# Kernel tuning notes

Hardware: AMD Instinct MI355X
Metric: run time of the kernel (lower is better)

The kernel has to match this reference:

```python
import jax, jax.numpy as jnp
import numpy as np

TOKENS, D_IN, D_OUT, N_FACTORS, RANK = 8192, 4096, 4096, 2, 64


def setup_inputs() -> dict:
    key = jax.random.key(0)
    ks = jax.random.split(key, 6)
    # kaiming_uniform-ish scales (exact init distribution is irrelevant for correctness)
    w_bound = 1.0 / np.sqrt(D_IN)
    x = jax.random.normal(ks[0], (TOKENS, D_IN), dtype=jnp.float32)
    W = jax.random.uniform(ks[1], (D_OUT, D_IN), jnp.float32, -w_bound, w_bound)
    bias = jax.random.uniform(ks[2], (D_OUT,), jnp.float32, -w_bound, w_bound)
    a_bound = 1.0 / np.sqrt(RANK)
    As = jax.random.uniform(ks[3], (N_FACTORS, D_OUT, RANK), jnp.float32, -a_bound, a_bound)
    Bs = jax.random.normal(ks[4], (N_FACTORS, RANK, RANK), dtype=jnp.float32) * 0.1
    # Cs initialized nonzero here so the low-rank path actually contributes
    Cs = jax.random.normal(ks[5], (N_FACTORS, RANK, D_IN), dtype=jnp.float32) * 0.02
    return {"x": x, "W": W, "bias": bias, "As": As, "Bs": Bs, "Cs": Cs}


def reference(x, W, bias, As, Bs, Cs):
    # W_eff = W + sum_f tanh(A_f) @ B_f @ C_f   (phi_A = tanh, B already transformed)
    # [f,o,r] x [f,r,k] -> [f,o,k]; then x [f,k,i] -> [o,i] summed over f
    AB = jnp.einsum('for,frk->fok', jnp.tanh(As), Bs)
    W_eff = W + jnp.einsum('fok,fki->oi', AB, Cs)
    # F.linear: x @ W_eff^T + bias
    return jnp.einsum('ti,oi->to', x, W_eff) + bias
```

## Files before the change

kernel.cpp:

```cpp
#include <hip/hip_runtime.h>
#include <hip/hip_bf16.h>

typedef __bf16 bf16x8 __attribute__((ext_vector_type(8)));
typedef float f32x4 __attribute__((ext_vector_type(4)));

#define TOKENS 8192
#define D_IN   4096
#define D_OUT  4096

static __device__ __forceinline__ unsigned short f2bf(float f) {
  union { float f; unsigned int u; } v; v.f = f;
  unsigned int r = v.u + 0x7FFFu + ((v.u >> 16) & 1u);
  return (unsigned short)(r >> 16);
}

__global__ void ab_kernel(const float* __restrict__ As,
                          const float* __restrict__ Bs,
                          float* __restrict__ ABt) {
  __shared__ float tA[4][64];
  __shared__ float sB[64][64];
  const int t = threadIdx.x;
  const int f = blockIdx.x >> 10;
  const int o0 = (blockIdx.x & 1023) * 4;
  const int ol = t >> 6;
  const int k  = t & 63;
  tA[ol][k] = tanhf(As[((size_t)f * 4096 + o0 + ol) * 64 + k]);
#pragma unroll
  for (int j = 0; j < 16; ++j) {
    int e = t + 256 * j;
    sB[e >> 6][e & 63] = Bs[f * 4096 + e];
  }
  __syncthreads();
  float acc = 0.f;
#pragma unroll
  for (int r = 0; r < 64; ++r) acc += tA[ol][r] * sB[r][k];
  ABt[(size_t)(o0 + ol) * 128 + f * 64 + k] = acc;
}

__global__ void weff_kernel(const float* __restrict__ W,
                            const float* __restrict__ ABt,
                            const float* __restrict__ Cs,
                            unsigned short* __restrict__ Weff) {
  __shared__ float sA[64][129];
  __shared__ float sB[32][64];
  const int t = threadIdx.x;
  const int i0 = blockIdx.x * 64;
  const int o0 = blockIdx.y * 64;
#pragma unroll
  for (int j = 0; j < 32; ++j) {
    int e = t + 256 * j;
    sA[e >> 7][e & 127] = ABt[(size_t)(o0 + (e >> 7)) * 128 + (e & 127)];
  }
  const int tx = t & 15, ty = t >> 4;
  float acc[4][4] = {};
  for (int kc = 0; kc < 128; kc += 32) {
    __syncthreads();
#pragma unroll
    for (int j = 0; j < 8; ++j) {
      int e = t + 256 * j;
      sB[e >> 6][e & 63] = Cs[(size_t)(kc + (e >> 6)) * D_IN + i0 + (e & 63)];
    }
    __syncthreads();
#pragma unroll
    for (int k = 0; k < 32; ++k) {
      float4 b = *(const float4*)&sB[k][tx * 4];
#pragma unroll
      for (int r = 0; r < 4; ++r) {
        float a = sA[ty * 4 + r][kc + k];
        acc[r][0] += a * b.x;
        acc[r][1] += a * b.y;
        acc[r][2] += a * b.z;
        acc[r][3] += a * b.w;
      }
    }
  }
#pragma unroll
  for (int r = 0; r < 4; ++r) {
    const int o = o0 + ty * 4 + r;
    const float4 w = *(const float4*)&W[(size_t)o * D_IN + i0 + tx * 4];
    union { unsigned short h[4]; uint2 u; } p;
    p.h[0] = f2bf(w.x + acc[r][0]);
    p.h[1] = f2bf(w.y + acc[r][1]);
    p.h[2] = f2bf(w.z + acc[r][2]);
    p.h[3] = f2bf(w.w + acc[r][3]);
    *(uint2*)(Weff + (size_t)o * D_IN + i0 + tx * 4) = p.u;
  }
}

__global__ void cast_kernel(const float* __restrict__ x,
                            unsigned short* __restrict__ xb) {
  size_t i = ((size_t)blockIdx.x * 256 + threadIdx.x) * 8;
  float4 a = *(const float4*)(x + i);
  float4 b = *(const float4*)(x + i + 4);
  union { unsigned short h[8]; uint4 u; } p;
  p.h[0] = f2bf(a.x); p.h[1] = f2bf(a.y);
  p.h[2] = f2bf(a.z); p.h[3] = f2bf(a.w);
  p.h[4] = f2bf(b.x); p.h[5] = f2bf(b.y);
  p.h[6] = f2bf(b.z); p.h[7] = f2bf(b.w);
  *(uint4*)(xb + i) = p.u;
}

__global__ __launch_bounds__(256) void gemm_kernel(
    const unsigned short* __restrict__ Abf,
    const unsigned short* __restrict__ Bbf,
    const float* __restrict__ bias,
    float* __restrict__ C) {
  const int K = D_IN, N = D_OUT;
  __shared__ __align__(16) unsigned short sA[128 * 64];
  __shared__ __align__(16) unsigned short sB[128 * 64];
  const int t = threadIdx.x;
  const int lane = t & 63;
  const int wave = t >> 6;
  const int bn = blockIdx.x, bm = blockIdx.y;
  const int wm = (wave & 1) * 64, wn = (wave >> 1) * 64;

  const int r8 = (t >> 3) & 7;
  const int cg = (t & 7) ^ r8;
  const unsigned short* ag = Abf + (size_t)(bm * 128 + (t >> 3)) * K + cg * 8;
  const unsigned short* bg = Bbf + (size_t)(bn * 128 + (t >> 3)) * K + cg * 8;
  unsigned short* la = sA + t * 8;
  unsigned short* lb = sB + t * 8;

  f32x4 acc[4][4] = {};
  const int lm = lane & 15;
  const int cb = lane >> 4;
  const int sw = lm & 7;

  for (int kt = 0; kt < K; kt += 64) {
    __syncthreads();
#pragma unroll
    for (int j = 0; j < 4; ++j) {
      __builtin_amdgcn_global_load_lds(
          (const __attribute__((address_space(1))) void*)(ag + (size_t)j * 32 * K + kt),
          (__attribute__((address_space(3))) void*)(la + j * 2048), 16, 0, 0);
      __builtin_amdgcn_global_load_lds(
          (const __attribute__((address_space(1))) void*)(bg + (size_t)j * 32 * K + kt),
          (__attribute__((address_space(3))) void*)(lb + j * 2048), 16, 0, 0);
    }
    __syncthreads();
#pragma unroll
    for (int ks = 0; ks < 2; ++ks) {
      const int ch = ((ks * 4 + cb) ^ sw) * 8;
      bf16x8 af[4], bfr[4];
#pragma unroll
      for (int mi = 0; mi < 4; ++mi)
        af[mi] = *(const bf16x8*)(sA + (wm + mi * 16 + lm) * 64 + ch);
#pragma unroll
      for (int ni = 0; ni < 4; ++ni)
        bfr[ni] = *(const bf16x8*)(sB + (wn + ni * 16 + lm) * 64 + ch);
#pragma unroll
      for (int mi = 0; mi < 4; ++mi)
#pragma unroll
        for (int ni = 0; ni < 4; ++ni)
          acc[mi][ni] = __builtin_amdgcn_mfma_f32_16x16x32_bf16(
              af[mi], bfr[ni], acc[mi][ni], 0, 0, 0);
    }
  }

  const int cn = lane & 15;
  const int rm = (lane >> 4) * 4;
#pragma unroll
  for (int ni = 0; ni < 4; ++ni) {
    const int col = bn * 128 + wn + ni * 16 + cn;
    const float bv = bias[col];
#pragma unroll
    for (int mi = 0; mi < 4; ++mi) {
      const int row0 = bm * 128 + wm + mi * 16 + rm;
#pragma unroll
      for (int r = 0; r < 4; ++r)
        C[(size_t)(row0 + r) * N + col] = acc[mi][ni][r] + bv;
    }
  }
}

extern "C" void kernel_launch(void* const* d_in, const int* in_sizes, int n_in,
                              void* d_out, int out_size, void* d_ws, size_t ws_size,
                              hipStream_t stream) {
  const float* x    = (const float*)d_in[0];
  const float* W    = (const float*)d_in[1];
  const float* bias = (const float*)d_in[2];
  const float* As   = (const float*)d_in[3];
  const float* Bs   = (const float*)d_in[4];
  const float* Cs   = (const float*)d_in[5];
  float* out = (float*)d_out;

  char* ws = (char*)d_ws;
  float* ABt           = (float*)ws;
  unsigned short* Weff = (unsigned short*)(ws + (2u << 20));
  unsigned short* xb   = (unsigned short*)(ws + (2u << 20) + (32u << 20));

  ab_kernel<<<2048, 256, 0, stream>>>(As, Bs, ABt);
  weff_kernel<<<dim3(64, 64), 256, 0, stream>>>(W, ABt, Cs, Weff);
  cast_kernel<<<16384, 256, 0, stream>>>(x, xb);
  gemm_kernel<<<dim3(32, 64), 256, 0, stream>>>(xb, Weff, bias, out);
}
```

Baseline: 600.2 us.

## Rewrite bf16 GEMM as 256x256 tile, 8-wave, double-buffered pipelined kernel

Replaces the 128x128 single-buffered GEMM with a 256x256 tile computed by 8 waves, double-buffered LDS, and interleaved global-to-LDS prefetches issued between MFMA quadrants with explicit waitcnt, barriers and setprio. It also adds workgroup-index swizzling for L2 locality. The goal is to hide global load latency behind MFMA work and raise arithmetic intensity per tile. In exchange it uses more LDS (128KB) and registers and depends on hand-tuned wait counts for correctness.

New measurement: 570.0 us. 5.0% less time.

```diff
diff --git a/kernel.cpp b/kernel.cpp
--- a/kernel.cpp
+++ b/kernel.cpp
@@ -100,72 +100,210 @@
   *(uint4*)(xb + i) = p.u;
 }
 
-__global__ __launch_bounds__(256) void gemm_kernel(
+
+#define FENCE()   asm volatile("" ::: "memory")
+#define BARRIER() do { FENCE(); __builtin_amdgcn_s_barrier(); FENCE(); } while (0)
+#define WAITLGKM() asm volatile("s_waitcnt lgkmcnt(0)" ::: "memory")
+#define WAITVM(n)  asm volatile("s_waitcnt vmcnt(" #n ")" ::: "memory")
+#define SCHEDB()   __builtin_amdgcn_sched_barrier(0)
+
+#define GLOAD(gptr, lptr)                                                     \
+  __builtin_amdgcn_global_load_lds(                                           \
+      (const __attribute__((address_space(1))) void*)(gptr),                  \
+      (__attribute__((address_space(3))) void*)(lptr), 16, 0, 0)
+
+#define STAGE_A(buf, h, kt) do {                                              \
+    GLOAD(ag + (size_t)((h) * 128) * K + (kt),                                \
+          lA + (buf) * 16384 + (h) * 8192);                                   \
+    GLOAD(ag + (size_t)((h) * 128 + 64) * K + (kt),                           \
+          lA + (buf) * 16384 + (h) * 8192 + 4096);                            \
+  } while (0)
+#define STAGE_B(buf, h, kt) do {                                              \
+    GLOAD(bg + (size_t)((h) * 128) * K + (kt),                                \
+          lB + (buf) * 16384 + (h) * 8192);                                   \
+    GLOAD(bg + (size_t)((h) * 128 + 64) * K + (kt),                           \
+          lB + (buf) * 16384 + (h) * 8192 + 4096);                            \
+  } while (0)
+
+#define LDA(buf, mi, ks) \
+  (*(const bf16x8*)(rA + (buf) * 16384 + (mi) * 1024 + ((ks) ? ch1 : ch0)))
+#define LDB(buf, ni, ks) \
+  (*(const bf16x8*)(rB + (buf) * 16384 + (ni) * 1024 + ((ks) ? ch1 : ch0)))
+
+#define MFMA1(d, a, b) \
+  (d) = __builtin_amdgcn_mfma_f32_16x16x32_bf16((a), (b), (d), 0, 0, 0)
+
+#define QUADRANT(q, A00, A01, A10, A11)                                       \
+    MFMA1(acc[2*(q)  ][0], A00, b00);                                         \
+    MFMA1(acc[2*(q)+1][0], A10, b00);                                         \
+    MFMA1(acc[2*(q)  ][1], A00, b10);                                         \
+    MFMA1(acc[2*(q)+1][1], A10, b10);                                         \
+    MFMA1(acc[2*(q)  ][2], A00, b20);                                         \
+    MFMA1(acc[2*(q)+1][2], A10, b20);                                         \
+    MFMA1(acc[2*(q)  ][3], A00, b30);                                         \
+    MFMA1(acc[2*(q)+1][3], A10, b30);                                         \
+    MFMA1(acc[2*(q)  ][0], A01, b01);                                         \
+    MFMA1(acc[2*(q)+1][0], A11, b01);                                         \
+    MFMA1(acc[2*(q)  ][1], A01, b11);                                         \
+    MFMA1(acc[2*(q)+1][1], A11, b11);                                         \
+    MFMA1(acc[2*(q)  ][2], A01, b21);                                         \
+    MFMA1(acc[2*(q)+1][2], A11, b21);                                         \
+    MFMA1(acc[2*(q)  ][3], A01, b31);                                         \
+    MFMA1(acc[2*(q)+1][3], A11, b31);
+
+#define GEMM_BODY(S2, S3, kt)                                                 \
+  {                                                                           \
+    bf16x8 b00, b01, b10, b11, b20, b21, b30, b31;                            \
+                        \
+    {                                                                 \
+      bf16x8 a00 = LDA(0, 0, 0), a01 = LDA(0, 0, 1);                          \
+      bf16x8 a10 = LDA(0, 1, 0), a11 = LDA(0, 1, 1);                          \
+      b00 = LDB(0, 0, 0); b01 = LDB(0, 0, 1);                                 \
+      b10 = LDB(0, 1, 0); b11 = LDB(0, 1, 1);                                 \
+      b20 = LDB(0, 2, 0); b21 = LDB(0, 2, 1);                                 \
+      b30 = LDB(0, 3, 0); b31 = LDB(0, 3, 1);                                 \
+      STAGE_A(1, 0, (kt) + 64);                                               \
+      BARRIER(); WAITLGKM(); SCHEDB();                                        \
+      __builtin_amdgcn_s_setprio(1);                                          \
+      QUADRANT(0, a00, a01, a10, a11);                                        \
+      __builtin_amdgcn_s_setprio(0);                                          \
+      BARRIER();                                                              \
+    }                                                                         \
+    {                                                                 \
+      bf16x8 a00 = LDA(0, 2, 0), a01 = LDA(0, 2, 1);                          \
+      bf16x8 a10 = LDA(0, 3, 0), a11 = LDA(0, 3, 1);                          \
+      STAGE_A(1, 1, (kt) + 64);                                               \
+      if (S2) STAGE_B(0, 0, (kt) + 128);                                      \
+      BARRIER(); WAITLGKM(); SCHEDB();                                        \
+      __builtin_amdgcn_s_setprio(1);                                          \
+      QUADRANT(1, a00, a01, a10, a11);                                        \
+      __builtin_amdgcn_s_setprio(0);                                          \
+      BARRIER();                                                              \
+    }                                                                         \
+    {                                                                 \
+      bf16x8 a00 = LDA(0, 4, 0), a01 = LDA(0, 4, 1);                          \
+      bf16x8 a10 = LDA(0, 5, 0), a11 = LDA(0, 5, 1);                          \
+      if (S2) STAGE_B(0, 1, (kt) + 128);                                      \
+      BARRIER(); WAITLGKM(); SCHEDB();                                        \
+      __builtin_amdgcn_s_setprio(1);                                          \
+      QUADRANT(2, a00, a01, a10, a11);                                        \
+      __builtin_amdgcn_s_setprio(0);                                          \
+      BARRIER();                                                              \
+    }                                                                         \
+    {                                                                 \
+      bf16x8 a00 = LDA(0, 6, 0), a01 = LDA(0, 6, 1);                          \
+      bf16x8 a10 = LDA(0, 7, 0), a11 = LDA(0, 7, 1);                          \
+      BARRIER(); WAITLGKM(); SCHEDB();                                        \
+      __builtin_amdgcn_s_setprio(1);                                          \
+      QUADRANT(3, a00, a01, a10, a11);                                        \
+      __builtin_amdgcn_s_setprio(0);                                          \
+      if (S2) { WAITVM(4); } else { WAITVM(0); }                              \
+      BARRIER();                                                              \
+    }                                                                         \
+                      \
+    {                                                                 \
+      bf16x8 a00 = LDA(1, 0, 0), a01 = LDA(1, 0, 1);                          \
+      bf16x8 a10 = LDA(1, 1, 0), a11 = LDA(1, 1, 1);                          \
+      b00 = LDB(1, 0, 0); b01 = LDB(1, 0, 1);                                 \
+      b10 = LDB(1, 1, 0); b11 = LDB(1, 1, 1);                                 \
+      b20 = LDB(1, 2, 0); b21 = LDB(1, 2, 1);                                 \
+      b30 = LDB(1, 3, 0); b31 = LDB(1, 3, 1);                                 \
+      if (S2) STAGE_A(0, 0, (kt) + 128);                                      \
+      BARRIER(); WAITLGKM(); SCHEDB();                                        \
+      __builtin_amdgcn_s_setprio(1);                                          \
+      QUADRANT(0, a00, a01, a10, a11);                                        \
+      __builtin_amdgcn_s_setprio(0);                                          \
+      BARRIER();                                                              \
+    }                                                                         \
+    {                                                                 \
+      bf16x8 a00 = LDA(1, 2, 0), a01 = LDA(1, 2, 1);                          \
+      bf16x8 a10 = LDA(1, 3, 0), a11 = LDA(1, 3, 1);                          \
+      if (S2) STAGE_A(0, 1, (kt) + 128);                                      \
+      if (S3) STAGE_B(1, 0, (kt) + 192);                                      \
+      BARRIER(); WAITLGKM(); SCHEDB();                                        \
+      __builtin_amdgcn_s_setprio(1);                                          \
+      QUADRANT(1, a00, a01, a10, a11);                                        \
+      __builtin_amdgcn_s_setprio(0);                                          \
+      BARRIER();                                                              \
+    }                                                                         \
+    {                                                                 \
+      bf16x8 a00 = LDA(1, 4, 0), a01 = LDA(1, 4, 1);                          \
+      bf16x8 a10 = LDA(1, 5, 0), a11 = LDA(1, 5, 1);                          \
+      if (S3) STAGE_B(1, 1, (kt) + 192);                                      \
+      BARRIER(); WAITLGKM(); SCHEDB();                                        \
+      __builtin_amdgcn_s_setprio(1);                                          \
+      QUADRANT(2, a00, a01, a10, a11);                                        \
+      __builtin_amdgcn_s_setprio(0);                                          \
+      BARRIER();                                                              \
+    }                                                                         \
+    {                                                                 \
+      bf16x8 a00 = LDA(1, 6, 0), a01 = LDA(1, 6, 1);                          \
+      bf16x8 a10 = LDA(1, 7, 0), a11 = LDA(1, 7, 1);                          \
+      BARRIER(); WAITLGKM(); SCHEDB();                                        \
+      __builtin_amdgcn_s_setprio(1);                                          \
+      QUADRANT(3, a00, a01, a10, a11);                                        \
+      __builtin_amdgcn_s_setprio(0);                                          \
+      if (S3) { WAITVM(4); } else { WAITVM(0); }                              \
+      BARRIER();                                                              \
+    }                                                                         \
+  }
+
+__global__ __launch_bounds__(512, 2) void gemm_kernel(
     const unsigned short* __restrict__ Abf,
     const unsigned short* __restrict__ Bbf,
     const float* __restrict__ bias,
     float* __restrict__ C) {
   const int K = D_IN, N = D_OUT;
-  __shared__ __align__(16) unsigned short sA[128 * 64];
-  __shared__ __align__(16) unsigned short sB[128 * 64];
+  __shared__ __align__(16) unsigned short sA[2 * 256 * 64];
+  __shared__ __align__(16) unsigned short sB[2 * 256 * 64];
   const int t = threadIdx.x;
   const int lane = t & 63;
   const int wave = t >> 6;
-  const int bn = blockIdx.x, bm = blockIdx.y;
-  const int wm = (wave & 1) * 64, wn = (wave >> 1) * 64;
-
-  const int r8 = (t >> 3) & 7;
-  const int cg = (t & 7) ^ r8;
-  const unsigned short* ag = Abf + (size_t)(bm * 128 + (t >> 3)) * K + cg * 8;
-  const unsigned short* bg = Bbf + (size_t)(bn * 128 + (t >> 3)) * K + cg * 8;
-  unsigned short* la = sA + t * 8;
-  unsigned short* lb = sB + t * 8;
-
-  f32x4 acc[4][4] = {};
+
+  const int wgid = blockIdx.y * gridDim.x + blockIdx.x;
+  const int swz = (wgid & 7) * 64 + (wgid >> 3);
+  const int bn = swz & 15;
+  const int bm = swz >> 4;
+
+  const int wm = (wave >> 2) * 128;
+  const int wn = (wave & 3) * 64;
+
+  const int tr = t >> 3;
+  const int cg = (t & 7) ^ (tr & 7);
+  const unsigned short* ag = Abf + (size_t)(bm * 256 + tr) * K + cg * 8;
+  const unsigned short* bg = Bbf + (size_t)(bn * 256 + tr) * K + cg * 8;
+  unsigned short* const lA = sA + t * 8;
+  unsigned short* const lB = sB + t * 8;
+
   const int lm = lane & 15;
   const int cb = lane >> 4;
   const int sw = lm & 7;
-
-  for (int kt = 0; kt < K; kt += 64) {
-    __syncthreads();
-#pragma unroll
-    for (int j = 0; j < 4; ++j) {
-      __builtin_amdgcn_global_load_lds(
-          (const __attribute__((address_space(1))) void*)(ag + (size_t)j * 32 * K + kt),
-          (__attribute__((address_space(3))) void*)(la + j * 2048), 16, 0, 0);
-      __builtin_amdgcn_global_load_lds(
-          (const __attribute__((address_space(1))) void*)(bg + (size_t)j * 32 * K + kt),
-          (__attribute__((address_space(3))) void*)(lb + j * 2048), 16, 0, 0);
-    }
-    __syncthreads();
-#pragma unroll
-    for (int ks = 0; ks < 2; ++ks) {
-      const int ch = ((ks * 4 + cb) ^ sw) * 8;
-      bf16x8 af[4], bfr[4];
-#pragma unroll
-      for (int mi = 0; mi < 4; ++mi)
-        af[mi] = *(const bf16x8*)(sA + (wm + mi * 16 + lm) * 64 + ch);
-#pragma unroll
-      for (int ni = 0; ni < 4; ++ni)
-        bfr[ni] = *(const bf16x8*)(sB + (wn + ni * 16 + lm) * 64 + ch);
-#pragma unroll
-      for (int mi = 0; mi < 4; ++mi)
-#pragma unroll
-        for (int ni = 0; ni < 4; ++ni)
-          acc[mi][ni] = __builtin_amdgcn_mfma_f32_16x16x32_bf16(
-              af[mi], bfr[ni], acc[mi][ni], 0, 0, 0);
-    }
-  }
+  const int ch0 = ((cb) ^ sw) * 8;
+  const int ch1 = ((4 + cb) ^ sw) * 8;
+  const unsigned short* rA = sA + (wm + lm) * 64;
+  const unsigned short* rB = sB + (wn + lm) * 64;
+
+  f32x4 acc[8][4] = {};
+
+  STAGE_B(0, 0, 0); STAGE_B(0, 1, 0);
+  STAGE_A(0, 0, 0); STAGE_A(0, 1, 0);
+  STAGE_B(1, 0, 64); STAGE_B(1, 1, 64);
+  WAITVM(4);
+  BARRIER();
+
+#pragma unroll 1
+  for (int kt = 0; kt < K - 128; kt += 128) GEMM_BODY(1, 1, kt)
+  GEMM_BODY(0, 0, K - 128)
 
   const int cn = lane & 15;
   const int rm = (lane >> 4) * 4;
 #pragma unroll
   for (int ni = 0; ni < 4; ++ni) {
-    const int col = bn * 128 + wn + ni * 16 + cn;
+    const int col = bn * 256 + wn + ni * 16 + cn;
     const float bv = bias[col];
 #pragma unroll
-    for (int mi = 0; mi < 4; ++mi) {
-      const int row0 = bm * 128 + wm + mi * 16 + rm;
+    for (int mi = 0; mi < 8; ++mi) {
+      const int row0 = bm * 256 + wm + mi * 16 + rm;
 #pragma unroll
       for (int r = 0; r < 4; ++r)
         C[(size_t)(row0 + r) * N + col] = acc[mi][ni][r] + bv;
@@ -192,5 +330,5 @@
   ab_kernel<<<2048, 256, 0, stream>>>(As, Bs, ABt);
   weff_kernel<<<dim3(64, 64), 256, 0, stream>>>(W, ABt, Cs, Weff);
   cast_kernel<<<16384, 256, 0, stream>>>(x, xb);
-  gemm_kernel<<<dim3(32, 64), 256, 0, stream>>>(xb, Weff, bias, out);
-}
+  gemm_kernel<<<dim3(16, 32), 512, 0, stream>>>(xb, Weff, bias, out);
+}
```

## Rewrite GEMM as 256x256 tile, 8-wave, double-buffered pipelined MFMA kernel

Applied to the files above, without the earlier changes.

Replaces the 128x128 single-buffered bf16 GEMM with a 256x256 tile processed by 512 threads. The LDS buffers are double-buffered and global-to-LDS loads are interleaved with MFMA quads through explicit barriers, vmcnt waits, sched barriers and setprio. Workgroup IDs are remapped for L2 locality. The aim is to hide global load latency and raise MFMA utilization. In exchange it uses 128KB of LDS and many registers, and the hand-scheduled waits and barriers are fragile.

Result: faster. 565.5 us (-5.8%).

```diff
diff --git a/kernel.cpp b/kernel.cpp
--- a/kernel.cpp
+++ b/kernel.cpp
@@ -100,72 +100,183 @@
   *(uint4*)(xb + i) = p.u;
 }
 
-__global__ __launch_bounds__(256) void gemm_kernel(
+
+#define FENCE()   asm volatile("" ::: "memory")
+#define BARRIER() do { FENCE(); __builtin_amdgcn_s_barrier(); FENCE(); } while (0)
+#define WAITVM(n)  asm volatile("s_waitcnt vmcnt(" #n ")" ::: "memory")
+#define SCHEDB()   __builtin_amdgcn_sched_barrier(0)
+#define PRIO1      __builtin_amdgcn_s_setprio(1)
+#define PRIO0      __builtin_amdgcn_s_setprio(0)
+
+#define GLOAD(gptr, lptr)                                                     \
+  __builtin_amdgcn_global_load_lds(                                           \
+      (const __attribute__((address_space(1))) void*)(gptr),                  \
+      (__attribute__((address_space(3))) void*)(lptr), 16, 0, 0)
+
+#define STAGE_A(buf, h, kt) do {                                              \
+    GLOAD(ag + (size_t)((h) * 128) * K + (kt),                                \
+          lA + (buf) * 16384 + (h) * 8192);                                   \
+    GLOAD(ag + (size_t)((h) * 128 + 64) * K + (kt),                           \
+          lA + (buf) * 16384 + (h) * 8192 + 4096);                            \
+  } while (0)
+#define STAGE_B(buf, h, kt) do {                                              \
+    GLOAD(bg + (size_t)((h) * 128) * K + (kt),                                \
+          lB + (buf) * 16384 + (h) * 8192);                                   \
+    GLOAD(bg + (size_t)((h) * 128 + 64) * K + (kt),                           \
+          lB + (buf) * 16384 + (h) * 8192 + 4096);                            \
+  } while (0)
+
+#define LDA(buf, mi, ks) \
+  (*(const bf16x8*)(rA + (buf) * 16384 + (mi) * 1024 + ((ks) ? ch1 : ch0)))
+#define LDB(buf, ni, ks) \
+  (*(const bf16x8*)(rB + (buf) * 16384 + (ni) * 1024 + ((ks) ? ch1 : ch0)))
+
+#define READ_A(R0, R1, R2, R3, buf, mi0) do {                                 \
+    R0 = LDA(buf, (mi0), 0);                                                  \
+    R2 = LDA(buf, (mi0) + 1, 0);                                              \
+    R1 = LDA(buf, (mi0), 1);                                                  \
+    R3 = LDA(buf, (mi0) + 1, 1);                                              \
+  } while (0)
+#define READ_B(buf) do {                                                      \
+    b00 = LDB(buf, 0, 0); b10 = LDB(buf, 1, 0);                               \
+    b20 = LDB(buf, 2, 0); b30 = LDB(buf, 3, 0);                               \
+    b01 = LDB(buf, 0, 1); b11 = LDB(buf, 1, 1);                               \
+    b21 = LDB(buf, 2, 1); b31 = LDB(buf, 3, 1);                               \
+  } while (0)
+
+#define MFMA1(d, a, b) \
+  (d) = __builtin_amdgcn_mfma_f32_16x16x32_bf16((a), (b), (d), 0, 0, 0)
+
+#define QUAD(q, A0, A1, A2, A3)                                               \
+    MFMA1(acc[2*(q)  ][0], A0, b00);                                          \
+    MFMA1(acc[2*(q)+1][0], A2, b00);                                          \
+    MFMA1(acc[2*(q)  ][1], A0, b10);                                          \
+    MFMA1(acc[2*(q)+1][1], A2, b10);                                          \
+    MFMA1(acc[2*(q)  ][2], A0, b20);                                          \
+    MFMA1(acc[2*(q)+1][2], A2, b20);                                          \
+    MFMA1(acc[2*(q)  ][3], A0, b30);                                          \
+    MFMA1(acc[2*(q)+1][3], A2, b30);                                          \
+    MFMA1(acc[2*(q)  ][0], A1, b01);                                          \
+    MFMA1(acc[2*(q)+1][0], A3, b01);                                          \
+    MFMA1(acc[2*(q)  ][1], A1, b11);                                          \
+    MFMA1(acc[2*(q)+1][1], A3, b11);                                          \
+    MFMA1(acc[2*(q)  ][2], A1, b21);                                          \
+    MFMA1(acc[2*(q)+1][2], A3, b21);                                          \
+    MFMA1(acc[2*(q)  ][3], A1, b31);                                          \
+    MFMA1(acc[2*(q)+1][3], A3, b31);
+
+#define GEMM_BODY(S2, S3, kt)                                                 \
+  {                                                                           \
+                             \
+    READ_B(0);                                                                \
+    READ_A(qa0, qa1, qa2, qa3, 0, 2);                                         \
+    STAGE_A(1, 0, (kt) + 64); STAGE_A(1, 1, (kt) + 64);                       \
+    BARRIER(); SCHEDB();                                                      \
+    PRIO1; QUAD(0, pa0, pa1, pa2, pa3); PRIO0; SCHEDB();                      \
+    BARRIER();                                                                \
+                                          \
+    READ_A(pa0, pa1, pa2, pa3, 0, 4);                                         \
+    if (S2) { STAGE_B(0, 0, (kt) + 128); STAGE_B(0, 1, (kt) + 128); }         \
+    BARRIER(); SCHEDB();                                                      \
+    PRIO1; QUAD(1, qa0, qa1, qa2, qa3); PRIO0; SCHEDB();                      \
+    BARRIER();                                                                \
+                         \
+    READ_A(qa0, qa1, qa2, qa3, 0, 6);                                         \
+    BARRIER(); SCHEDB();                                                      \
+    PRIO1; QUAD(2, pa0, pa1, pa2, pa3); PRIO0; SCHEDB();                      \
+    if (S2) { WAITVM(4); } else { WAITVM(0); }                                \
+    BARRIER();                                                                \
+                                  \
+    READ_A(pa0, pa1, pa2, pa3, 1, 0);                                         \
+    BARRIER(); SCHEDB();                                                      \
+    PRIO1; QUAD(3, qa0, qa1, qa2, qa3); PRIO0; SCHEDB();                      \
+    BARRIER();                                                                \
+                               \
+    READ_B(1);                                                                \
+    READ_A(qa0, qa1, qa2, qa3, 1, 2);                                         \
+    if (S2) { STAGE_A(0, 0, (kt) + 128); STAGE_A(0, 1, (kt) + 128); }         \
+    BARRIER(); SCHEDB();                                                      \
+    PRIO1; QUAD(0, pa0, pa1, pa2, pa3); PRIO0; SCHEDB();                      \
+    BARRIER();                                                                \
+                                        \
+    READ_A(pa0, pa1, pa2, pa3, 1, 4);                                         \
+    if (S3) { STAGE_B(1, 0, (kt) + 192); STAGE_B(1, 1, (kt) + 192); }         \
+    BARRIER(); SCHEDB();                                                      \
+    PRIO1; QUAD(1, qa0, qa1, qa2, qa3); PRIO0; SCHEDB();                      \
+    BARRIER();                                                                \
+                       \
+    READ_A(qa0, qa1, qa2, qa3, 1, 6);                                         \
+    BARRIER(); SCHEDB();                                                      \
+    PRIO1; QUAD(2, pa0, pa1, pa2, pa3); PRIO0; SCHEDB();                      \
+    if (S3) { WAITVM(4); } else { WAITVM(0); }                                \
+    BARRIER();                                                                \
+                                  \
+    if (S2) { READ_A(pa0, pa1, pa2, pa3, 0, 0); }                             \
+    BARRIER(); SCHEDB();                                                      \
+    PRIO1; QUAD(3, qa0, qa1, qa2, qa3); PRIO0; SCHEDB();                      \
+    BARRIER();                                                                \
+  }
+
+__global__ __launch_bounds__(512, 2) void gemm_kernel(
     const unsigned short* __restrict__ Abf,
     const unsigned short* __restrict__ Bbf,
     const float* __restrict__ bias,
     float* __restrict__ C) {
   const int K = D_IN, N = D_OUT;
-  __shared__ __align__(16) unsigned short sA[128 * 64];
-  __shared__ __align__(16) unsigned short sB[128 * 64];
+  __shared__ __align__(16) unsigned short sA[2 * 256 * 64];
+  __shared__ __align__(16) unsigned short sB[2 * 256 * 64];
   const int t = threadIdx.x;
   const int lane = t & 63;
   const int wave = t >> 6;
-  const int bn = blockIdx.x, bm = blockIdx.y;
-  const int wm = (wave & 1) * 64, wn = (wave >> 1) * 64;
-
-  const int r8 = (t >> 3) & 7;
-  const int cg = (t & 7) ^ r8;
-  const unsigned short* ag = Abf + (size_t)(bm * 128 + (t >> 3)) * K + cg * 8;
-  const unsigned short* bg = Bbf + (size_t)(bn * 128 + (t >> 3)) * K + cg * 8;
-  unsigned short* la = sA + t * 8;
-  unsigned short* lb = sB + t * 8;
-
-  f32x4 acc[4][4] = {};
+
+  const int wgid = blockIdx.y * gridDim.x + blockIdx.x;
+  const int swz = (wgid & 7) * 64 + (wgid >> 3);
+  const int bn = swz & 15;
+  const int bm = swz >> 4;
+
+  const int wm = (wave >> 2) * 128;
+  const int wn = (wave & 3) * 64;
+
+  const int tr = t >> 3;
+  const int cg = (t & 7) ^ (tr & 7);
+  const unsigned short* ag = Abf + (size_t)(bm * 256 + tr) * K + cg * 8;
+  const unsigned short* bg = Bbf + (size_t)(bn * 256 + tr) * K + cg * 8;
+  unsigned short* const lA = sA + t * 8;
+  unsigned short* const lB = sB + t * 8;
+
   const int lm = lane & 15;
   const int cb = lane >> 4;
   const int sw = lm & 7;
-
-  for (int kt = 0; kt < K; kt += 64) {
-    __syncthreads();
-#pragma unroll
-    for (int j = 0; j < 4; ++j) {
-      __builtin_amdgcn_global_load_lds(
-          (const __attribute__((address_space(1))) void*)(ag + (size_t)j * 32 * K + kt),
-          (__attribute__((address_space(3))) void*)(la + j * 2048), 16, 0, 0);
-      __builtin_amdgcn_global_load_lds(
-          (const __attribute__((address_space(1))) void*)(bg + (size_t)j * 32 * K + kt),
-          (__attribute__((address_space(3))) void*)(lb + j * 2048), 16, 0, 0);
-    }
-    __syncthreads();
-#pragma unroll
-    for (int ks = 0; ks < 2; ++ks) {
-      const int ch = ((ks * 4 + cb) ^ sw) * 8;
-      bf16x8 af[4], bfr[4];
-#pragma unroll
-      for (int mi = 0; mi < 4; ++mi)
-        af[mi] = *(const bf16x8*)(sA + (wm + mi * 16 + lm) * 64 + ch);
-#pragma unroll
-      for (int ni = 0; ni < 4; ++ni)
-        bfr[ni] = *(const bf16x8*)(sB + (wn + ni * 16 + lm) * 64 + ch);
-#pragma unroll
-      for (int mi = 0; mi < 4; ++mi)
-#pragma unroll
-        for (int ni = 0; ni < 4; ++ni)
-          acc[mi][ni] = __builtin_amdgcn_mfma_f32_16x16x32_bf16(
-              af[mi], bfr[ni], acc[mi][ni], 0, 0, 0);
-    }
-  }
+  const int ch0 = ((cb) ^ sw) * 8;
+  const int ch1 = ((4 + cb) ^ sw) * 8;
+  const unsigned short* rA = sA + (wm + lm) * 64;
+  const unsigned short* rB = sB + (wn + lm) * 64;
+
+  f32x4 acc[8][4] = {};
+  bf16x8 pa0, pa1, pa2, pa3;
+  bf16x8 qa0, qa1, qa2, qa3;
+  bf16x8 b00, b10, b20, b30, b01, b11, b21, b31;
+
+  STAGE_B(0, 0, 0); STAGE_B(0, 1, 0);
+  STAGE_A(0, 0, 0); STAGE_A(0, 1, 0);
+  STAGE_B(1, 0, 64); STAGE_B(1, 1, 64);
+  WAITVM(4);
+  BARRIER();
+  READ_A(pa0, pa1, pa2, pa3, 0, 0);
+
+#pragma unroll 1
+  for (int kt = 0; kt < K - 128; kt += 128) GEMM_BODY(1, 1, kt)
+  GEMM_BODY(0, 0, K - 128)
 
   const int cn = lane & 15;
   const int rm = (lane >> 4) * 4;
 #pragma unroll
   for (int ni = 0; ni < 4; ++ni) {
-    const int col = bn * 128 + wn + ni * 16 + cn;
+    const int col = bn * 256 + wn + ni * 16 + cn;
     const float bv = bias[col];
 #pragma unroll
-    for (int mi = 0; mi < 4; ++mi) {
-      const int row0 = bm * 128 + wm + mi * 16 + rm;
+    for (int mi = 0; mi < 8; ++mi) {
+      const int row0 = bm * 256 + wm + mi * 16 + rm;
 #pragma unroll
       for (int r = 0; r < 4; ++r)
         C[(size_t)(row0 + r) * N + col] = acc[mi][ni][r] + bv;
@@ -192,5 +303,5 @@
   ab_kernel<<<2048, 256, 0, stream>>>(As, Bs, ABt);
   weff_kernel<<<dim3(64, 64), 256, 0, stream>>>(W, ABt, Cs, Weff);
   cast_kernel<<<16384, 256, 0, stream>>>(x, xb);
-  gemm_kernel<<<dim3(32, 64), 256, 0, stream>>>(xb, Weff, bias, out);
-}
+  gemm_kernel<<<dim3(16, 32), 512, 0, stream>>>(xb, Weff, bias, out);
+}
```
